# Kernel optimization log

Measured on AMD Instinct MI355X. Metric: run time of the kernel, lower is better.

The kernel has to match this reference:

```python
import jax, jax.numpy as jnp
import numpy as np

B, L, D = 2, 2048, 2048
H, G, E = 16, 4, 128       # num_heads, group_num, head dim
KV = H // G                # kv heads = 4
OUT = D                    # output_dim == input_dim for residual


def setup_inputs() -> dict:
    key = jax.random.key(0)
    ks = jax.random.split(key, 12)
    s_in = 1.0 / np.sqrt(D)
    s_o = 1.0 / np.sqrt(H * E)
    return {
        "x": jax.random.normal(ks[0], (B, L, D), jnp.float32),
        "Wq": jax.random.normal(ks[1], (D, H * E), jnp.float32) * s_in,
        "bq": jnp.zeros((H * E,), jnp.float32),
        "Wk": jax.random.normal(ks[2], (D, KV * E), jnp.float32) * s_in,
        "bk": jnp.zeros((KV * E,), jnp.float32),
        "Wv": jax.random.normal(ks[3], (D, KV * E), jnp.float32) * s_in,
        "bv": jnp.zeros((KV * E,), jnp.float32),
        "Wo": jax.random.normal(ks[4], (H * E, OUT), jnp.float32) * s_o,
        "bo": jnp.zeros((OUT,), jnp.float32),
        "gamma": jnp.ones((OUT,), jnp.float32),
        "beta": jnp.zeros((OUT,), jnp.float32),
    }


def reference(x, Wq, bq, Wk, bk, Wv, bv, Wo, bo, gamma, beta):
    b, l, _ = x.shape
    Q = (x @ Wq + bq).reshape(b, l, H, E)            # [B,L,H,E]
    K = (x @ Wk + bk).reshape(b, l, KV, E)           # [B,L,KV,E]
    V = (x @ Wv + bv).reshape(b, l, KV, E)
    # GQA expand: reshape(B,L,1,KV,E).expand(G) -> head h = g*KV + kv (tile kv heads G times)
    K = jnp.broadcast_to(K[:, :, None, :, :], (b, l, G, KV, E)).reshape(b, l, H, E)
    V = jnp.broadcast_to(V[:, :, None, :, :], (b, l, G, KV, E)).reshape(b, l, H, E)
    scores = jnp.einsum('blhe,bmhe->bhlm', Q, K) / np.sqrt(E).astype(np.float32)
    # causal mask: triu(ones, diag=1) * -1e9 added to scores
    mask = jnp.triu(jnp.ones((l, l), jnp.float32), k=1) * (-1e9)
    attn = jax.nn.softmax(scores + mask[None, None, :, :], axis=-1)
    ctx = jnp.einsum('bhlm,bmhe->blhe', attn, V).reshape(b, l, H * E)
    y = jax.nn.gelu(ctx @ Wo + bo, approximate=False)  # nn.GELU default = exact erf
    r = x + y
    mu = jnp.mean(r, axis=-1, keepdims=True)
    var = jnp.var(r, axis=-1, keepdims=True)
    return (r - mu) * jax.lax.rsqrt(var + 1e-5) * gamma + beta
```

## Files before the change

kernel.cpp:

```cpp
#include <hip/hip_runtime.h>
#include <hip/hip_bf16.h>
#include <math.h>

typedef __bf16 bf16_t;
typedef __bf16 bf16x4 __attribute__((ext_vector_type(4)));
typedef __bf16 bf16x8 __attribute__((ext_vector_type(8)));
typedef float  f32x4  __attribute__((ext_vector_type(4)));
typedef float  f32x16 __attribute__((ext_vector_type(16)));

#define MFMA16(a,b,c) __builtin_amdgcn_mfma_f32_16x16x32_bf16((a),(b),(c),0,0,0)
#define MFMA32(a,b,c) __builtin_amdgcn_mfma_f32_32x32x16_bf16((a),(b),(c),0,0,0)

#define B_ 2
#define L_ 2048
#define D_ 2048
#define H_ 16
#define KV_ 4
#define E_ 128
#define M_ (B_*L_)
#define NQKV_ 3072

__device__ __forceinline__ void async_ld16(const bf16_t* g, bf16_t* l) {
    __builtin_amdgcn_global_load_lds((const __attribute__((address_space(1))) void*)g,
                                     (__attribute__((address_space(3))) void*)l, 16, 0, 0);
}

__global__ __launch_bounds__(256) void cast_bias_kernel(const float* __restrict__ src,
                                                        bf16_t* __restrict__ dst,
                                                        const float* __restrict__ bq,
                                                        const float* __restrict__ bk,
                                                        const float* __restrict__ bv,
                                                        float* __restrict__ qbias) {
    int bid = blockIdx.x;
    if (bid < 8192) {
        int i = (bid * 256 + threadIdx.x) * 4;
        float4 v = *(const float4*)(src + i);
        bf16x4 o;
        o.x = (bf16_t)v.x; o.y = (bf16_t)v.y; o.z = (bf16_t)v.z; o.w = (bf16_t)v.w;
        *(bf16x4*)(dst + i) = o;
    } else {
        int i = (bid - 8192) * 256 + threadIdx.x;
        if (i < 2048) qbias[i] = bq[i];
        else if (i < 2560) qbias[i] = bk[i - 2048];
        else if (i < 3072) qbias[i] = bv[i - 2560];
    }
}

__global__ __launch_bounds__(256) void wtrans_kernel(const float* __restrict__ Wq,
                                                     const float* __restrict__ Wk,
                                                     const float* __restrict__ Wv,
                                                     const float* __restrict__ Wo,
                                                     bf16_t* __restrict__ WqkvT,
                                                     bf16_t* __restrict__ WoT) {
    __shared__ float tile[32][33];
    int bx = blockIdx.x;
    const float* W; bf16_t* WT; int N, n0;
    if (bx < 64)      { W = Wq; WT = WqkvT;                  N = 2048; n0 = bx * 32; }
    else if (bx < 80) { W = Wk; WT = WqkvT + 2048 * 2048;    N = 512;  n0 = (bx - 64) * 32; }
    else if (bx < 96) { W = Wv; WT = WqkvT + 2560 * 2048;    N = 512;  n0 = (bx - 80) * 32; }
    else              { W = Wo; WT = WoT;                    N = 2048; n0 = (bx - 96) * 32; }
    int k0 = blockIdx.y * 32;
    int tx = threadIdx.x, ty = threadIdx.y;
    #pragma unroll
    for (int i = 0; i < 32; i += 8)
        tile[ty + i][tx] = W[(size_t)(k0 + ty + i) * N + n0 + tx];
    __syncthreads();
    #pragma unroll
    for (int i = 0; i < 32; i += 8)
        WT[(size_t)(n0 + ty + i) * 2048 + k0 + tx] = (bf16_t)tile[tx][ty + i];
}

__global__ __launch_bounds__(256) void transpose_v_kernel(const bf16_t* __restrict__ QKV,
                                                          bf16_t* __restrict__ Vt) {
    __shared__ bf16_t tile[32][33];
    int e0 = blockIdx.x * 32, l0 = blockIdx.y * 32;
    int bk = blockIdx.z;
    int b = bk >> 2, kv = bk & 3;
    int tx = threadIdx.x, ty = threadIdx.y;
    #pragma unroll
    for (int i = 0; i < 32; i += 8)
        tile[ty + i][tx] = QKV[(size_t)(b * L_ + l0 + ty + i) * NQKV_ + 2560 + kv * 128 + e0 + tx];
    __syncthreads();
    #pragma unroll
    for (int i = 0; i < 32; i += 8)
        Vt[((size_t)bk * 128 + e0 + ty + i) * L_ + l0 + tx] = tile[tx][ty + i];
}

template <bool OUT_BF16, bool GELU>
__global__ __launch_bounds__(256) void gemm_kernel(const bf16_t* __restrict__ A,
                                                   const bf16_t* __restrict__ BT,
                                                   const float* __restrict__ bias,
                                                   void* __restrict__ C,
                                                   int M, int N, int K) {
    __shared__ __align__(16) bf16_t sA[128][32];
    __shared__ __align__(16) bf16_t sB[128][32];
    int tid = threadIdx.x;
    int wave = tid >> 6, lane = tid & 63;
    int l16 = lane & 15, quad = lane >> 4;
    int row0 = blockIdx.y * 128;
    int col0 = blockIdx.x * 128;
    int wm = (wave >> 1) * 64;
    int wn = (wave & 1) * 64;

    f32x4 acc[4][4];
    #pragma unroll
    for (int i = 0; i < 4; ++i)
        #pragma unroll
        for (int j = 0; j < 4; ++j)
            acc[i][j] = f32x4{0.f, 0.f, 0.f, 0.f};

    for (int k0 = 0; k0 < K; k0 += 32) {
        #pragma unroll
        for (int c = 0; c < 2; ++c) {
            int lin = (c * 256 + tid) * 8;
            int r = lin >> 5, col = lin & 31;
            async_ld16(&A[(size_t)(row0 + r) * K + k0 + col], &sA[r][col]);
            async_ld16(&BT[(size_t)(col0 + r) * K + k0 + col], &sB[r][col]);
        }
        __syncthreads();
        bf16x8 af[4], bf[4];
        #pragma unroll
        for (int mt = 0; mt < 4; ++mt) af[mt] = *(const bf16x8*)&sA[wm + mt * 16 + l16][quad * 8];
        #pragma unroll
        for (int nt = 0; nt < 4; ++nt) bf[nt] = *(const bf16x8*)&sB[wn + nt * 16 + l16][quad * 8];
        #pragma unroll
        for (int mt = 0; mt < 4; ++mt)
            #pragma unroll
            for (int nt = 0; nt < 4; ++nt)
                acc[mt][nt] = MFMA16(af[mt], bf[nt], acc[mt][nt]);
        __syncthreads();
    }

    #pragma unroll
    for (int mt = 0; mt < 4; ++mt) {
        #pragma unroll
        for (int nt = 0; nt < 4; ++nt) {
            int gcol = col0 + wn + nt * 16 + l16;
            float bv = bias[gcol];
            #pragma unroll
            for (int r = 0; r < 4; ++r) {
                int grow = row0 + wm + mt * 16 + quad * 4 + r;
                float v = acc[mt][nt][r] + bv;
                if (GELU) v = 0.5f * v * (1.f + erff(v * 0.70710678118654752f));
                if (OUT_BF16) ((bf16_t*)C)[(size_t)grow * N + gcol] = (bf16_t)v;
                else          ((float*)C)[(size_t)grow * N + gcol] = v;
            }
        }
    }
}

__global__ __launch_bounds__(256) void attn_kernel(const bf16_t* __restrict__ QKV,
                                                   const bf16_t* __restrict__ Vt,
                                                   bf16_t* __restrict__ Ctx) {
    __shared__ __align__(16) bf16_t sK[2][64][128];
    __shared__ __align__(16) bf16_t sV[2][128][64];

    const int tid = threadIdx.x;
    const int wave = tid >> 6, lane = tid & 63;
    const int unit = wave >> 1, wv = wave & 1;
    const int l31 = lane & 31, half = lane >> 5;
    const int pair = blockIdx.x & 15;
    const int h = (blockIdx.x >> 4) & 15;
    const int b = blockIdx.x >> 8;
    const int kv = h & 3;

    const bf16_t* Kbase = QKV + (size_t)b * L_ * NQKV_ + 2048 + kv * 128;
    const bf16_t* Vbase = Vt + (size_t)(b * 4 + kv) * 128 * L_;
    const float scale = 0.08838834764831845f;

    const int t_u = unit ? 31 - pair : pair;
    const int ktmax = 31 - pair;
    const int qrow = t_u * 64 + wv * 32 + l31;

    bf16x8 qf[8];
    const bf16_t* Qrow = QKV + (size_t)(b * L_ + qrow) * NQKV_ + h * 128 + half * 8;
    #pragma unroll
    for (int et = 0; et < 8; ++et) qf[et] = *(const bf16x8*)&Qrow[et * 16];

    f32x16 acc[4];
    #pragma unroll
    for (int em = 0; em < 4; ++em)
        #pragma unroll
        for (int j = 0; j < 16; ++j) acc[em][j] = 0.f;
    float m_i = -3.0e38f, l_i = 0.f;

    bf16x8 kreg[4], vreg[4];
    #define LOAD_TILE(KT)                                                            \
        {                                                                            \
            int kk = (KT) * 64;                                                      \
            _Pragma("unroll")                                                        \
            for (int p = 0; p < 4; ++p) {                                            \
                int ch = p * 256 + tid;                                              \
                int rk = ch >> 4, ck = ch & 15;                                      \
                kreg[p] = *(const bf16x8*)&Kbase[(size_t)(kk + rk) * NQKV_ + ck * 8];\
                int rv = ch >> 3, cv = ch & 7;                                       \
                vreg[p] = *(const bf16x8*)&Vbase[(size_t)rv * L_ + kk + cv * 8];     \
            }                                                                        \
        }

    LOAD_TILE(0);

    for (int kt = 0; kt <= ktmax; ++kt) {
        const int bufi = kt & 1;
        #pragma unroll
        for (int p = 0; p < 4; ++p) {
            int ch = p * 256 + tid;
            int rk = ch >> 4, ck = ch & 15;
            *(bf16x8*)&sK[bufi][rk][(ck ^ (rk & 15)) * 8] = kreg[p];
            int rv = ch >> 3, cv = ch & 7;
            *(bf16x8*)&sV[bufi][rv][(cv ^ (rv & 7)) * 8] = vreg[p];
        }
        __syncthreads();
        if (kt < ktmax) LOAD_TILE(kt + 1);

        if (kt <= t_u) {
            f32x16 s[2];
            #pragma unroll
            for (int mt = 0; mt < 2; ++mt)
                #pragma unroll
                for (int j = 0; j < 16; ++j) s[mt][j] = 0.f;
            #pragma unroll
            for (int mt = 0; mt < 2; ++mt)
                #pragma unroll
                for (int et = 0; et < 8; ++et) {
                    bf16x8 kf = *(const bf16x8*)&sK[bufi][mt * 32 + l31][((et * 2 + half) ^ (l31 & 15)) * 8];
                    s[mt] = MFMA32(kf, qf[et], s[mt]);
                }

            #pragma unroll
            for (int mt = 0; mt < 2; ++mt)
                #pragma unroll
                for (int j = 0; j < 16; ++j) s[mt][j] *= scale;

            if (kt == t_u) {
                #pragma unroll
                for (int mt = 0; mt < 2; ++mt)
                    #pragma unroll
                    for (int j = 0; j < 16; ++j) {
                        int kidx = kt * 64 + mt * 32 + (j & 3) + 8 * (j >> 2) + 4 * half;
                        if (kidx > qrow) s[mt][j] = -3.0e38f;
                    }
            }

            float mx = s[0][0];
            #pragma unroll
            for (int mt = 0; mt < 2; ++mt)
                #pragma unroll
                for (int j = 0; j < 16; ++j) mx = fmaxf(mx, s[mt][j]);
            mx = fmaxf(mx, __shfl_xor(mx, 32, 64));
            float mnew = fmaxf(m_i, mx);
            float alpha = __expf(m_i - mnew);
            float rs = 0.f;
            #pragma unroll
            for (int mt = 0; mt < 2; ++mt)
                #pragma unroll
                for (int j = 0; j < 16; ++j) {
                    float p = __expf(s[mt][j] - mnew);
                    s[mt][j] = p;
                    rs += p;
                }
            rs += __shfl_xor(rs, 32, 64);
            l_i = l_i * alpha + rs;
            m_i = mnew;
            #pragma unroll
            for (int em = 0; em < 4; ++em)
                #pragma unroll
                for (int j = 0; j < 16; ++j) acc[em][j] *= alpha;

            bf16x4 pk[2][4];
            #pragma unroll
            for (int mt = 0; mt < 2; ++mt)
                #pragma unroll
                for (int g = 0; g < 4; ++g) {
                    bf16x4 t;
                    #pragma unroll
                    for (int i = 0; i < 4; ++i) t[i] = (bf16_t)s[mt][g * 4 + i];
                    pk[mt][g] = t;
                }

            #pragma unroll
            for (int kc = 0; kc < 4; ++kc) {
                const int mts = kc >> 1, g0 = 2 * (kc & 1);
                bf16x4 send = half ? pk[mts][g0] : pk[mts][g0 + 1];
                bf16x4 keep = half ? pk[mts][g0 + 1] : pk[mts][g0];
                union { bf16x4 v; int i[2]; } su, ru;
                su.v = send;
                ru.i[0] = __shfl_xor(su.i[0], 32, 64);
                ru.i[1] = __shfl_xor(su.i[1], 32, 64);
                bf16x4 lo = half ? ru.v : keep;
                bf16x4 hi = half ? keep : ru.v;
                bf16x8 pf = __builtin_shufflevector(lo, hi, 0, 1, 2, 3, 4, 5, 6, 7);
                #pragma unroll
                for (int em = 0; em < 4; ++em) {
                    bf16x8 vf = *(const bf16x8*)&sV[bufi][em * 32 + l31][((kc * 2 + half) ^ (l31 & 7)) * 8];
                    acc[em] = MFMA32(vf, pf, acc[em]);
                }
            }
        }
    }

    const float inv = 1.f / l_i;
    bf16_t* Cp = Ctx + (size_t)(b * L_ + qrow) * 2048 + h * 128;
    #pragma unroll
    for (int em = 0; em < 4; ++em)
        #pragma unroll
        for (int g = 0; g < 4; ++g) {
            bf16x4 ov;
            #pragma unroll
            for (int i = 0; i < 4; ++i) ov[i] = (bf16_t)(acc[em][g * 4 + i] * inv);
            *(bf16x4*)&Cp[em * 32 + g * 8 + half * 4] = ov;
        }
}

__global__ __launch_bounds__(256) void ln_kernel(const bf16_t* __restrict__ Y,
                                                 const float* __restrict__ X,
                                                 const float* __restrict__ gamma,
                                                 const float* __restrict__ beta,
                                                 float* __restrict__ out) {
    __shared__ float sr[2048];
    __shared__ float wred[8];
    size_t row = blockIdx.x;
    const bf16_t* y = Y + row * 2048;
    const float* x = X + row * 2048;
    float sum = 0.f, ssq = 0.f;
    #pragma unroll
    for (int c = 0; c < 2; ++c) {
        int i = (c * 256 + threadIdx.x) * 4;
        bf16x4 yv = *(const bf16x4*)(y + i);
        float4 xv = *(const float4*)(x + i);
        float r0 = xv.x + (float)yv[0];
        float r1 = xv.y + (float)yv[1];
        float r2 = xv.z + (float)yv[2];
        float r3 = xv.w + (float)yv[3];
        sr[i] = r0; sr[i + 1] = r1; sr[i + 2] = r2; sr[i + 3] = r3;
        sum += r0 + r1 + r2 + r3;
        ssq += r0 * r0 + r1 * r1 + r2 * r2 + r3 * r3;
    }
    #pragma unroll
    for (int off = 32; off > 0; off >>= 1) {
        sum += __shfl_xor(sum, off, 64);
        ssq += __shfl_xor(ssq, off, 64);
    }
    int wv = threadIdx.x >> 6;
    if ((threadIdx.x & 63) == 0) { wred[wv] = sum; wred[wv + 4] = ssq; }
    __syncthreads();
    sum = wred[0] + wred[1] + wred[2] + wred[3];
    ssq = wred[4] + wred[5] + wred[6] + wred[7];
    float mu = sum * (1.f / 2048.f);
    float var = ssq * (1.f / 2048.f) - mu * mu;
    float rstd = rsqrtf(var + 1e-5f);
    #pragma unroll
    for (int c = 0; c < 2; ++c) {
        int i = (c * 256 + threadIdx.x) * 4;
        float4 gv = *(const float4*)(gamma + i);
        float4 bv = *(const float4*)(beta + i);
        float4 o;
        o.x = (sr[i]     - mu) * rstd * gv.x + bv.x;
        o.y = (sr[i + 1] - mu) * rstd * gv.y + bv.y;
        o.z = (sr[i + 2] - mu) * rstd * gv.z + bv.z;
        o.w = (sr[i + 3] - mu) * rstd * gv.w + bv.w;
        *(float4*)(out + row * 2048 + i) = o;
    }
}

extern "C" void kernel_launch(void* const* d_in, const int* in_sizes, int n_in,
                              void* d_out, int out_size, void* d_ws, size_t ws_size,
                              hipStream_t stream) {
    const float* x     = (const float*)d_in[0];
    const float* Wq    = (const float*)d_in[1];
    const float* bq    = (const float*)d_in[2];
    const float* Wk    = (const float*)d_in[3];
    const float* bk    = (const float*)d_in[4];
    const float* Wv    = (const float*)d_in[5];
    const float* bv    = (const float*)d_in[6];
    const float* Wo    = (const float*)d_in[7];
    const float* bo    = (const float*)d_in[8];
    const float* gamma = (const float*)d_in[9];
    const float* beta  = (const float*)d_in[10];
    float* out = (float*)d_out;

    char* ws = (char*)d_ws;
    size_t off = 0;
    bf16_t* xb    = (bf16_t*)(ws + off); off += 16777216;
    bf16_t* WqkvT = (bf16_t*)(ws + off); off += 12582912;
    bf16_t* WoT   = (bf16_t*)(ws + off); off += 8388608;
    float*  qbias = (float*)(ws + off);  off += 12288;
    bf16_t* QKV   = (bf16_t*)(ws + off); off += 25165824;
    bf16_t* Vt    = (bf16_t*)(ws + off); off += 4194304;
    bf16_t* Cb    = (bf16_t*)(ws + off); off += 16777216;
    bf16_t* Yb    = (bf16_t*)(ws + off); off += 16777216;

    cast_bias_kernel<<<8204, 256, 0, stream>>>(x, xb, bq, bk, bv, qbias);
    wtrans_kernel<<<dim3(160, 64), dim3(32, 8), 0, stream>>>(Wq, Wk, Wv, Wo, WqkvT, WoT);

    gemm_kernel<true, false><<<dim3(24, 32), 256, 0, stream>>>(xb, WqkvT, qbias, QKV, M_, NQKV_, D_);
    transpose_v_kernel<<<dim3(4, 64, 8), dim3(32, 8), 0, stream>>>(QKV, Vt);
    attn_kernel<<<512, 256, 0, stream>>>(QKV, Vt, Cb);
    gemm_kernel<true, true><<<dim3(16, 32), 256, 0, stream>>>(Cb, WoT, bo, Yb, M_, D_, 2048);
    ln_kernel<<<M_, 256, 0, stream>>>(Yb, x, gamma, beta, out);
}
```

Baseline: 389.8 us.

## Restructure attention blocks to 128-row query tiles with lazy softmax rescale

Each attention block now owns one contiguous 128-row query tile, replacing the paired short/long causal tiles. Blocks are ordered so the longest tiles launch first. The four waves share K/V tiles, and the loop runs until the tile's last diagonal block. Softmax folds the scale into a single exp2 FMA and only rescales the accumulator when the running max grows by more than a threshold. MFMA sections are wrapped in s_setprio. The cost is idle waves on the final diagonal tile, plus bounded-growth numerics from the lazy rescale.

```diff
diff --git a/kernel.cpp b/kernel.cpp
--- a/kernel.cpp
+++ b/kernel.cpp
@@ -157,20 +157,22 @@
 
     const int tid = threadIdx.x;
     const int wave = tid >> 6, lane = tid & 63;
-    const int unit = wave >> 1, wv = wave & 1;
     const int l31 = lane & 31, half = lane >> 5;
-    const int pair = blockIdx.x & 15;
-    const int h = (blockIdx.x >> 4) & 15;
-    const int b = blockIdx.x >> 8;
+
+    const int idx = blockIdx.x;
+    const int r = idx >> 5;
+    const int bh = idx & 31;
+    const int t = (r < 8) ? (15 - r) : (r - 8);
+    const int h = bh & 15, b = bh >> 4;
     const int kv = h & 3;
 
     const bf16_t* Kbase = QKV + (size_t)b * L_ * NQKV_ + 2048 + kv * 128;
     const bf16_t* Vbase = Vt + (size_t)(b * 4 + kv) * 128 * L_;
-    const float scale = 0.08838834764831845f;
-
-    const int t_u = unit ? 31 - pair : pair;
-    const int ktmax = 31 - pair;
-    const int qrow = t_u * 64 + wv * 32 + l31;
+    const float SC = 0.12754995f;
+
+    const int qrow = t * 128 + wave * 32 + l31;
+    const int ktlast = 2 * t + 1;
+    const int ktmax_w = 2 * t + (wave >> 1);
 
     bf16x8 qf[8];
     const bf16_t* Qrow = QKV + (size_t)(b * L_ + qrow) * NQKV_ + h * 128 + half * 8;
@@ -182,7 +184,7 @@
     for (int em = 0; em < 4; ++em)
         #pragma unroll
         for (int j = 0; j < 16; ++j) acc[em][j] = 0.f;
-    float m_i = -3.0e38f, l_i = 0.f;
+    float m_i = -3.0e38f, l_i = 0.f, nmb = 0.f;
 
     bf16x8 kreg[4], vreg[4];
     #define LOAD_TILE(KT)                                                            \
@@ -200,7 +202,7 @@
 
     LOAD_TILE(0);
 
-    for (int kt = 0; kt <= ktmax; ++kt) {
+    for (int kt = 0; kt <= ktlast; ++kt) {
         const int bufi = kt & 1;
         #pragma unroll
         for (int p = 0; p < 4; ++p) {
@@ -211,14 +213,15 @@
             *(bf16x8*)&sV[bufi][rv][(cv ^ (rv & 7)) * 8] = vreg[p];
         }
         __syncthreads();
-        if (kt < ktmax) LOAD_TILE(kt + 1);
-
-        if (kt <= t_u) {
+        if (kt < ktlast) LOAD_TILE(kt + 1);
+
+        if (kt <= ktmax_w) {
             f32x16 s[2];
             #pragma unroll
             for (int mt = 0; mt < 2; ++mt)
                 #pragma unroll
                 for (int j = 0; j < 16; ++j) s[mt][j] = 0.f;
+            __builtin_amdgcn_s_setprio(1);
             #pragma unroll
             for (int mt = 0; mt < 2; ++mt)
                 #pragma unroll
@@ -226,13 +229,9 @@
                     bf16x8 kf = *(const bf16x8*)&sK[bufi][mt * 32 + l31][((et * 2 + half) ^ (l31 & 15)) * 8];
                     s[mt] = MFMA32(kf, qf[et], s[mt]);
                 }
-
-            #pragma unroll
-            for (int mt = 0; mt < 2; ++mt)
-                #pragma unroll
-                for (int j = 0; j < 16; ++j) s[mt][j] *= scale;
-
-            if (kt == t_u) {
+            __builtin_amdgcn_s_setprio(0);
+
+            if (kt == ktmax_w) {
                 #pragma unroll
                 for (int mt = 0; mt < 2; ++mt)
                     #pragma unroll
@@ -248,34 +247,38 @@
                 #pragma unroll
                 for (int j = 0; j < 16; ++j) mx = fmaxf(mx, s[mt][j]);
             mx = fmaxf(mx, __shfl_xor(mx, 32, 64));
-            float mnew = fmaxf(m_i, mx);
-            float alpha = __expf(m_i - mnew);
+            if (__any(mx > m_i + 64.f)) {
+                float mnew = fmaxf(m_i, mx);
+                float al = exp2f((m_i - mnew) * SC);
+                l_i *= al;
+                #pragma unroll
+                for (int em = 0; em < 4; ++em)
+                    #pragma unroll
+                    for (int j = 0; j < 16; ++j) acc[em][j] *= al;
+                m_i = mnew;
+                nmb = -m_i * SC;
+            }
             float rs = 0.f;
             #pragma unroll
             for (int mt = 0; mt < 2; ++mt)
                 #pragma unroll
                 for (int j = 0; j < 16; ++j) {
-                    float p = __expf(s[mt][j] - mnew);
+                    float p = exp2f(fmaf(s[mt][j], SC, nmb));
                     s[mt][j] = p;
                     rs += p;
                 }
             rs += __shfl_xor(rs, 32, 64);
-            l_i = l_i * alpha + rs;
-            m_i = mnew;
-            #pragma unroll
-            for (int em = 0; em < 4; ++em)
-                #pragma unroll
-                for (int j = 0; j < 16; ++j) acc[em][j] *= alpha;
+            l_i += rs;
 
             bf16x4 pk[2][4];
             #pragma unroll
             for (int mt = 0; mt < 2; ++mt)
                 #pragma unroll
                 for (int g = 0; g < 4; ++g) {
-                    bf16x4 t;
+                    bf16x4 tt;
                     #pragma unroll
-                    for (int i = 0; i < 4; ++i) t[i] = (bf16_t)s[mt][g * 4 + i];
-                    pk[mt][g] = t;
+                    for (int i = 0; i < 4; ++i) tt[i] = (bf16_t)s[mt][g * 4 + i];
+                    pk[mt][g] = tt;
                 }
 
             #pragma unroll
@@ -290,11 +293,13 @@
                 bf16x4 lo = half ? ru.v : keep;
                 bf16x4 hi = half ? keep : ru.v;
                 bf16x8 pf = __builtin_shufflevector(lo, hi, 0, 1, 2, 3, 4, 5, 6, 7);
+                __builtin_amdgcn_s_setprio(1);
                 #pragma unroll
                 for (int em = 0; em < 4; ++em) {
                     bf16x8 vf = *(const bf16x8*)&sV[bufi][em * 32 + l31][((kc * 2 + half) ^ (l31 & 7)) * 8];
                     acc[em] = MFMA32(vf, pf, acc[em]);
                 }
+                __builtin_amdgcn_s_setprio(0);
             }
         }
     }
```

Result: faster. 373.9 us (-4.1%).
